# Optimization experiments

Measured on AMD Instinct MI355X. Metric: run time of the kernel, lower is better.

## Reference

```python
import jax, jax.numpy as jnp
import numpy as np

DT_RANK = 64
N_STATES = 16


def selective_scan(u, delta, A, B, C, D):
    # u,delta: [b,l,d]; A: [d,n]; B,C: [b,l,n]; D: [d]
    dA = jnp.einsum('bld,dn->bldn', delta, A)
    dB_u = jnp.einsum('bld,bld,bln->bldn', delta, u, B)
    # shifted exclusive suffix-sum: cum[t] = sum_{s=t+1}^{L-1} dA[s]
    dA_shift = jnp.concatenate([dA[:, 1:], jnp.zeros_like(dA[:, :1])], axis=1)
    dA_cumsum = jnp.exp(jnp.flip(jnp.cumsum(jnp.flip(dA_shift, axis=1), axis=1), axis=1))
    xs = jnp.cumsum(dB_u * dA_cumsum, axis=1) / (dA_cumsum + 1e-12)
    y = jnp.einsum('bldn,bln->bld', xs, C)
    return y + u * D


def setup_inputs() -> dict:
    key = jax.random.key(0)
    ks = jax.random.split(key, 6)
    b, l, d = 2, 1024, 1024
    dt_rank, n = DT_RANK, N_STATES
    x = jax.random.normal(ks[0], (b, l, d), dtype=jnp.float32)
    # Dense kernels with glorot-ish scale
    W_x = jax.random.normal(ks[1], (d, dt_rank + 2 * n), dtype=jnp.float32) * (1.0 / np.sqrt(d))
    W_dt = jax.random.normal(ks[2], (dt_rank, d), dtype=jnp.float32) * (1.0 / np.sqrt(dt_rank))
    b_dt = jnp.zeros((d,), dtype=jnp.float32)
    # A_log = log(repeat(1..n, d)) as in S6.__init__
    A_log = jnp.log(jnp.tile(jnp.arange(1, n + 1, dtype=jnp.float32)[None, :], (d, 1)))
    D = jnp.ones((d,), dtype=jnp.float32)
    W_out = jax.random.normal(ks[3], (d, d), dtype=jnp.float32) * (1.0 / np.sqrt(d))
    b_out = jnp.zeros((d,), dtype=jnp.float32)
    return {"x": x, "W_x": W_x, "W_dt": W_dt, "b_dt": b_dt,
            "A_log": A_log, "D": D, "W_out": W_out, "b_out": b_out}


def reference(x, W_x, W_dt, b_dt, A_log, D, W_out, b_out):
    n = A_log.shape[1]
    A = -jnp.exp(A_log)                     # [d,n]
    x_dbl = jnp.einsum('bld,de->ble', x, W_x)  # [b,l,dt_rank+2n]
    delta = x_dbl[..., :DT_RANK]
    B = x_dbl[..., DT_RANK:DT_RANK + n]
    C = x_dbl[..., DT_RANK + n:]
    delta = jax.nn.softplus(jnp.einsum('blr,rd->bld', delta, W_dt) + b_dt)
    y = selective_scan(x, delta, A, B, C, D)
    return jnp.einsum('bld,de->ble', y, W_out) + b_out
```

## Files before the change

kernel.cpp:

```cpp
#include <hip/hip_runtime.h>
#include <hip/hip_bf16.h>

#define LSEQ 1024
#define DMODEL 1024
#define NSTATE 16
#define DTRANK 64
#define ECOL 96
#define MTOT 2048

typedef short s16x8 __attribute__((ext_vector_type(8)));
typedef float f32x4 __attribute__((ext_vector_type(4)));
typedef unsigned int u32x4 __attribute__((ext_vector_type(4)));

#if __has_builtin(__builtin_amdgcn_exp2f)
#define EXP2F(x) __builtin_amdgcn_exp2f(x)
#else
#define EXP2F(x) exp2f(x)
#endif
#define LOG2E 1.4426950408889634

__device__ inline unsigned short f2bf(float f) {
    unsigned int u = __builtin_bit_cast(unsigned int, f);
    u += 0x7FFFu + ((u >> 16) & 1u);
    return (unsigned short)(u >> 16);
}
__device__ inline float bf2f(unsigned short h) {
    unsigned int u = ((unsigned int)h) << 16;
    return __builtin_bit_cast(float, u);
}

__device__ inline f32x4 shflup4(f32x4 v, int off) {
    f32x4 r;
    r[0] = __shfl_up(v[0], off, 64);
    r[1] = __shfl_up(v[1], off, 64);
    r[2] = __shfl_up(v[2], off, 64);
    r[3] = __shfl_up(v[3], off, 64);
    return r;
}

__global__ __launch_bounds__(256) void k_prep(const float* __restrict__ x,
                                              const float* __restrict__ Wx,
                                              const float* __restrict__ Wdt,
                                              const float* __restrict__ Wout,
                                              unsigned short* __restrict__ xTbf,
                                              unsigned short* __restrict__ WxTh,
                                              unsigned short* __restrict__ WxTl,
                                              unsigned short* __restrict__ WdtTh,
                                              unsigned short* __restrict__ WdtTl,
                                              unsigned short* __restrict__ WbfT) {
    __shared__ float t[64][65];
    int id = blockIdx.x;
    int tid = threadIdx.x;
    if (id < 512) {
        int d0 = (id & 15) * 64, m0 = (id >> 4) * 64;
        int tx = tid & 63, ty = tid >> 6;
#pragma unroll
        for (int j = 0; j < 64; j += 4)
            t[ty + j][tx] = x[(size_t)(m0 + ty + j) * 1024 + d0 + tx];
        __syncthreads();
#pragma unroll
        for (int j = 0; j < 64; j += 4)
            xTbf[(size_t)(d0 + ty + j) * 2048 + m0 + tx] = f2bf(t[tx][ty + j]);
    } else if (id < 512 + 96) {
        int id2 = id - 512;
        int e0 = (id2 % 3) * 32, k0 = (id2 / 3) * 32;
        int tx = tid & 31, ty = tid >> 5;
#pragma unroll
        for (int j = 0; j < 32; j += 8)
            t[ty + j][tx] = Wx[(size_t)(k0 + ty + j) * 96 + e0 + tx];
        __syncthreads();
#pragma unroll
        for (int j = 0; j < 32; j += 8) {
            float v = t[tx][ty + j];
            unsigned short h = f2bf(v);
            WxTh[(size_t)(e0 + ty + j) * 1024 + k0 + tx] = h;
            WxTl[(size_t)(e0 + ty + j) * 1024 + k0 + tx] = f2bf(v - bf2f(h));
        }
    } else if (id < 512 + 96 + 64) {
        int id3 = id - (512 + 96);
        int d0 = (id3 & 31) * 32, r0 = (id3 >> 5) * 32;
        int tx = tid & 31, ty = tid >> 5;
#pragma unroll
        for (int j = 0; j < 32; j += 8)
            t[ty + j][tx] = Wdt[(size_t)(r0 + ty + j) * 1024 + d0 + tx];
        __syncthreads();
#pragma unroll
        for (int j = 0; j < 32; j += 8) {
            float v = t[tx][ty + j];
            unsigned short h = f2bf(v);
            WdtTh[(size_t)(d0 + ty + j) * 64 + r0 + tx] = h;
            WdtTl[(size_t)(d0 + ty + j) * 64 + r0 + tx] = f2bf(v - bf2f(h));
        }
    } else {
        int id4 = id - (512 + 96 + 64);
        int e0 = (id4 & 15) * 64, k0 = (id4 >> 4) * 64;
        int tx = tid & 63, ty = tid >> 6;
#pragma unroll
        for (int j = 0; j < 64; j += 4)
            t[ty + j][tx] = Wout[(size_t)(k0 + ty + j) * 1024 + e0 + tx];
        __syncthreads();
#pragma unroll
        for (int j = 0; j < 64; j += 4)
            WbfT[(size_t)(e0 + ty + j) * 1024 + k0 + tx] = f2bf(t[tx][ty + j]);
    }
}

__global__ __launch_bounds__(256) void k_xdbl3(const float* __restrict__ x,
                                               const unsigned short* __restrict__ WxTh,
                                               const unsigned short* __restrict__ WxTl,
                                               float* __restrict__ part) {
    __shared__ unsigned short Ah[32 * 64], Al[32 * 64];
    __shared__ unsigned short Bh[96 * 64], Bl[96 * 64];
    int bm = (blockIdx.x >> 2) * 32;
    int slice = blockIdx.x & 3;
    int tid = threadIdx.x, lane = tid & 63, w = tid >> 6;
    int wm = w >> 1, wn = w & 1;
    int r = lane & 15, kb = lane >> 4;

    f32x4 acc[3];
#pragma unroll
    for (int nf = 0; nf < 3; ++nf) acc[nf] = (f32x4){0.f, 0.f, 0.f, 0.f};

#pragma unroll 1
    for (int kc = 0; kc < 4; ++kc) {
        int kbase = slice * 256 + kc * 64;
        __syncthreads();
        {
            int row = tid >> 3, cc = tid & 7;
            size_t src = (size_t)(bm + row) * 1024 + kbase + cc * 8;
            float4 v0 = *(const float4*)&x[src];
            float4 v1 = *(const float4*)&x[src + 4];
            float vv[8] = {v0.x, v0.y, v0.z, v0.w, v1.x, v1.y, v1.z, v1.w};
            s16x8 h, lo;
#pragma unroll
            for (int j = 0; j < 8; ++j) {
                unsigned short hb = f2bf(vv[j]);
                h[j] = (short)hb;
                lo[j] = (short)f2bf(vv[j] - bf2f(hb));
            }
            int dstB = row * 128 + ((cc * 16) ^ ((row & 7) << 4));
            *(s16x8*)((char*)Ah + dstB) = h;
            *(s16x8*)((char*)Al + dstB) = lo;
        }
#pragma unroll
        for (int j = 0; j < 3; ++j) {
            int c = tid + j * 256;
            int row = c >> 3, cc = c & 7;
            size_t src = (size_t)row * 1024 + kbase + cc * 8;
            int dstB = row * 128 + ((cc * 16) ^ ((row & 7) << 4));
            *(s16x8*)((char*)Bh + dstB) = *(const s16x8*)&WxTh[src];
            *(s16x8*)((char*)Bl + dstB) = *(const s16x8*)&WxTl[src];
        }
        __syncthreads();
#pragma unroll
        for (int ks = 0; ks < 2; ++ks) {
            int sw = (ks * 64 + kb * 16) ^ ((r & 7) << 4);
            s16x8 a_h = *(const s16x8*)((char*)Ah + (wm * 16 + r) * 128 + sw);
            s16x8 a_l = *(const s16x8*)((char*)Al + (wm * 16 + r) * 128 + sw);
#pragma unroll
            for (int nf = 0; nf < 3; ++nf) {
                int brow = wn * 48 + nf * 16 + r;
                s16x8 b_h = *(const s16x8*)((char*)Bh + brow * 128 + sw);
                s16x8 b_l = *(const s16x8*)((char*)Bl + brow * 128 + sw);
                acc[nf] = __builtin_amdgcn_mfma_f32_16x16x32_bf16(a_h, b_h, acc[nf], 0, 0, 0);
                acc[nf] = __builtin_amdgcn_mfma_f32_16x16x32_bf16(a_h, b_l, acc[nf], 0, 0, 0);
                acc[nf] = __builtin_amdgcn_mfma_f32_16x16x32_bf16(a_l, b_h, acc[nf], 0, 0, 0);
            }
        }
    }
    float* pb = part + (size_t)slice * 2048 * 96;
#pragma unroll
    for (int nf = 0; nf < 3; ++nf)
#pragma unroll
        for (int j = 0; j < 4; ++j)
            pb[(size_t)(bm + wm * 16 + kb * 4 + j) * 96 + wn * 48 + nf * 16 + r] = acc[nf][j];
}

__global__ __launch_bounds__(256) void k_delta2(const float* __restrict__ part,
                                                const unsigned short* __restrict__ WdtTh,
                                                const unsigned short* __restrict__ WdtTl,
                                                const float* __restrict__ bdt,
                                                float* __restrict__ deltaT,
                                                float* __restrict__ bpk,
                                                float* __restrict__ cpk) {
    __shared__ char pool[34816];
    unsigned short* Ah = (unsigned short*)pool;
    unsigned short* Al = (unsigned short*)(pool + 16384);
    float (*slab)[32][68] = (float (*)[32][68])pool;

    int bm = blockIdx.y * 128;
    int bn = blockIdx.x * 64;
    int tid = threadIdx.x, lane = tid & 63, w = tid >> 6;
    int wm = w >> 1, wn = w & 1;
    int r = lane & 15, kb = lane >> 4;

#pragma unroll
    for (int i = 0; i < 8; ++i) {
        int q = tid + i * 256;
        int row = q >> 4, c4 = q & 15;
        size_t off = (size_t)(bm + row) * 96 + c4 * 4;
        f32x4 v = *(const f32x4*)&part[off];
#pragma unroll
        for (int s = 1; s < 4; ++s) v += *(const f32x4*)&part[(size_t)s * 2048 * 96 + off];
        ushort4 h4, l4;
        h4.x = f2bf(v[0]); l4.x = f2bf(v[0] - bf2f(h4.x));
        h4.y = f2bf(v[1]); l4.y = f2bf(v[1] - bf2f(h4.y));
        h4.z = f2bf(v[2]); l4.z = f2bf(v[2] - bf2f(h4.z));
        h4.w = f2bf(v[3]); l4.w = f2bf(v[3] - bf2f(h4.w));
        int dstB = row * 128 + ((c4 * 8) ^ ((row & 7) << 4));
        *(ushort4*)((char*)Ah + dstB) = h4;
        *(ushort4*)((char*)Al + dstB) = l4;
    }
    if (blockIdx.x == 0) {
#pragma unroll
        for (int i = 0; i < 4; ++i) {
            int q = tid + i * 256;
            int row = q >> 3, c4 = q & 7;
            size_t off = (size_t)(bm + row) * 96 + 64 + c4 * 4;
            f32x4 v = *(const f32x4*)&part[off];
#pragma unroll
            for (int s = 1; s < 4; ++s) v += *(const f32x4*)&part[(size_t)s * 2048 * 96 + off];
            if (c4 < 4) *(f32x4*)&bpk[(size_t)(bm + row) * 16 + c4 * 4] = v;
            else        *(f32x4*)&cpk[(size_t)(bm + row) * 16 + (c4 - 4) * 4] = v;
        }
    }
    __syncthreads();

    f32x4 acc[4][2];
#pragma unroll
    for (int mf = 0; mf < 4; ++mf)
#pragma unroll
        for (int nf = 0; nf < 2; ++nf) acc[mf][nf] = (f32x4){0.f, 0.f, 0.f, 0.f};

#pragma unroll
    for (int ks = 0; ks < 2; ++ks) {
        int sw = (ks * 64 + kb * 16) ^ ((r & 7) << 4);
        s16x8 Afh[4], Afl[4], Bh[2], Bl[2];
#pragma unroll
        for (int mf = 0; mf < 4; ++mf) {
            int arow = wm * 64 + mf * 16 + r;
            Afh[mf] = *(const s16x8*)((char*)Ah + arow * 128 + sw);
            Afl[mf] = *(const s16x8*)((char*)Al + arow * 128 + sw);
        }
#pragma unroll
        for (int nf = 0; nf < 2; ++nf) {
            size_t b = (size_t)(bn + wn * 32 + nf * 16 + r) * 64 + ks * 32 + kb * 8;
            Bh[nf] = *(const s16x8*)&WdtTh[b];
            Bl[nf] = *(const s16x8*)&WdtTl[b];
        }
#pragma unroll
        for (int mf = 0; mf < 4; ++mf)
#pragma unroll
            for (int nf = 0; nf < 2; ++nf) {
                acc[mf][nf] = __builtin_amdgcn_mfma_f32_16x16x32_bf16(Afh[mf], Bh[nf], acc[mf][nf], 0, 0, 0);
                acc[mf][nf] = __builtin_amdgcn_mfma_f32_16x16x32_bf16(Afh[mf], Bl[nf], acc[mf][nf], 0, 0, 0);
                acc[mf][nf] = __builtin_amdgcn_mfma_f32_16x16x32_bf16(Afl[mf], Bh[nf], acc[mf][nf], 0, 0, 0);
            }
    }
    __syncthreads();

#pragma unroll
    for (int nf = 0; nf < 2; ++nf) {
        float bb = bdt[bn + wn * 32 + nf * 16 + r];
#pragma unroll
        for (int mf = 0; mf < 4; ++mf)
#pragma unroll
            for (int j = 0; j < 4; ++j) {
                float z = acc[mf][nf][j] + bb;
                float sp = fmaxf(z, 0.f) + log1pf(expf(-fabsf(z)));
                slab[w][nf * 16 + r][mf * 16 + kb * 4 + j] = sp;
            }
    }
#pragma unroll
    for (int i = 0; i < 8; ++i) {
        int idx = i * 64 + lane;
        int dl = idx >> 4, mq = (idx & 15) * 4;
        f32x4 v = *(const f32x4*)&slab[w][dl][mq];
        *(f32x4*)&deltaT[(size_t)(bn + wn * 32 + dl) * MTOT + bm + wm * 64 + mq] = v;
    }
}

__global__ __launch_bounds__(256) void k_scan3(const float* __restrict__ deltaT,
                                               const unsigned short* __restrict__ xTbf,
                                               const float* __restrict__ bpk,
                                               const float* __restrict__ cpk,
                                               const float* __restrict__ Alog,
                                               const float* __restrict__ Dp,
                                               unsigned short* __restrict__ yTbf) {
    __shared__ double csum[64];
    __shared__ double Rbef[64];
    __shared__ float TcL[64 * 20];
    __shared__ float syp[64 * 17];

    int tid = threadIdx.x;
    int c = tid >> 2, l = tid & 3;
    int w = tid >> 6, lane = tid & 63;
    int d = blockIdx.x & 1023, b = blockIdx.x >> 10;
    int m0 = b * 1024;

    const f32x4* dp = (const f32x4*)(deltaT + (size_t)d * MTOT + m0 + c * 16);
    const unsigned short* up = xTbf + (size_t)d * MTOT + m0 + c * 16;
    const f32x4* Bp = (const f32x4*)bpk + (size_t)(m0 + c * 16) * 4 + l;
    const f32x4* Cp = (const f32x4*)cpk + (size_t)(m0 + c * 16) * 4 + l;

    double dsum = 0.0;
#pragma unroll
    for (int i = 0; i < 4; ++i) {
        f32x4 v = dp[i];
        dsum += (double)v[0] + (double)v[1] + (double)v[2] + (double)v[3];
    }
    if (l == 0) csum[c] = dsum;
    __syncthreads();
    if (tid < 64) {
        double v = csum[tid];
#pragma unroll
        for (int off = 1; off < 64; off <<= 1) {
            double t = __shfl_down(v, off, 64);
            if (tid + off < 64) v += t;
        }
        Rbef[tid] = v;
    }
    __syncthreads();

    float Af2[4], Sb2[4];
    double Rb = Rbef[c];
#pragma unroll
    for (int j = 0; j < 4; ++j) {
        float Af = -__expf(Alog[d * NSTATE + 4 * l + j]);
        double A2 = (double)Af * LOG2E;
        Af2[j] = (float)A2;
        Sb2[j] = (float)(A2 * Rb);
    }
    float Dv = Dp[d];

    float P = 0.f;
    f32x4 Tn = {0.f, 0.f, 0.f, 0.f};
#pragma unroll 1
    for (int t4 = 0; t4 < 4; ++t4) {
        f32x4 rdv = dp[t4];
        ushort4 uv = *(const ushort4*)(up + t4 * 4);
        float ru[4] = {bf2f(uv.x), bf2f(uv.y), bf2f(uv.z), bf2f(uv.w)};
        f32x4 Bq[4];
#pragma unroll
        for (int k = 0; k < 4; ++k) Bq[k] = Bp[(t4 * 4 + k) * 4];
#pragma unroll
        for (int k = 0; k < 4; ++k) {
            float dlt = rdv[k];
            P += dlt;
            float du = dlt * ru[k];
#pragma unroll
            for (int j = 0; j < 4; ++j) {
                float e = EXP2F(fmaf(-Af2[j], P, Sb2[j]));
                Tn[j] = fmaf(du * Bq[k][j], e, Tn[j]);
            }
        }
    }
    *(f32x4*)&TcL[c * 20 + 4 * l] = Tn;
    __syncthreads();

    {
        f32x4 v = *(const f32x4*)&TcL[lane * 20 + 4 * w];
#pragma unroll
        for (int off = 1; off < 64; off <<= 1) {
            f32x4 t = shflup4(v, off);
            if (lane >= off) v += t;
        }
        f32x4 ex = shflup4(v, 1);
        if (lane == 0) ex = (f32x4){0.f, 0.f, 0.f, 0.f};
        *(f32x4*)&TcL[lane * 20 + 4 * w] = ex;
    }
    __syncthreads();
    f32x4 num = *(const f32x4*)&TcL[c * 20 + 4 * l];

    P = 0.f;
#pragma unroll 1
    for (int t4 = 0; t4 < 4; ++t4) {
        f32x4 rdv = dp[t4];
        ushort4 uv = *(const ushort4*)(up + t4 * 4);
        float ru[4] = {bf2f(uv.x), bf2f(uv.y), bf2f(uv.z), bf2f(uv.w)};
        f32x4 Bq[4], Cq[4];
#pragma unroll
        for (int k = 0; k < 4; ++k) {
            Bq[k] = Bp[(t4 * 4 + k) * 4];
            Cq[k] = Cp[(t4 * 4 + k) * 4];
        }
#pragma unroll
        for (int k = 0; k < 4; ++k) {
            float dlt = rdv[k];
            P += dlt;
            float du = dlt * ru[k];
            float psum = 0.f;
#pragma unroll
            for (int j = 0; j < 4; ++j) {
                float e = EXP2F(fmaf(-Af2[j], P, Sb2[j]));
                num[j] = fmaf(du * Bq[k][j], e, num[j]);
                float rr = __builtin_amdgcn_rcpf(e + 1e-12f);
                psum = fmaf(num[j] * rr, Cq[k][j], psum);
            }
            psum += __shfl_xor(psum, 1);
            psum += __shfl_xor(psum, 2);
            if (l == 0) syp[c * 17 + t4 * 4 + k] = fmaf(ru[k], Dv, psum);
        }
    }
    __syncthreads();
    {
        int cc = tid >> 2, oo = (tid & 3) * 4;
        const float* sp = &syp[cc * 17 + oo];
        ushort4 o;
        o.x = f2bf(sp[0]);
        o.y = f2bf(sp[1]);
        o.z = f2bf(sp[2]);
        o.w = f2bf(sp[3]);
        *reinterpret_cast<ushort4*>(&yTbf[(size_t)d * MTOT + m0 + tid * 4]) = o;
    }
}

__global__ __launch_bounds__(256) void k_gemm(const unsigned short* __restrict__ yT,
                                              const unsigned short* __restrict__ B,
                                              const float* __restrict__ bias,
                                              float* __restrict__ out) {
    __shared__ unsigned int P[32 * 68];
    __shared__ unsigned short Bs[64 * 64];
    const int GN = 1024, GK = 1024;
    int bm = blockIdx.y * 64;
    int bn = blockIdx.x * 64;
    int tid = threadIdx.x;
    int lane = tid & 63;
    int w = tid >> 6;
    int wm = w >> 1, wn = w & 1;
    int r = lane & 15, kb = lane >> 4;

    f32x4 acc[2][2];
#pragma unroll
    for (int mf = 0; mf < 2; ++mf)
#pragma unroll
        for (int nf = 0; nf < 2; ++nf) acc[mf][nf] = (f32x4){0.f, 0.f, 0.f, 0.f};

    ushort4 rya[2], ryb[2];
    s16x8 rbv[2];
    auto stage_load = [&](int k0) {
#pragma unroll
        for (int i = 0; i < 2; ++i) {
            int slot = tid + i * 256;
            int p = slot >> 4, mq = (slot & 15) * 4;
            rya[i] = *(const ushort4*)&yT[(size_t)(k0 + 2 * p) * MTOT + bm + mq];
            ryb[i] = *(const ushort4*)&yT[(size_t)(k0 + 2 * p + 1) * MTOT + bm + mq];
            rbv[i] = *(const s16x8*)&B[(size_t)(bn + (slot >> 3)) * GK + k0 + (slot & 7) * 8];
        }
    };

    stage_load(0);
    for (int k0 = 0; k0 < GK; k0 += 64) {
        __syncthreads();
#pragma unroll
        for (int i = 0; i < 2; ++i) {
            int slot = tid + i * 256;
            int p = slot >> 4, mq = (slot & 15) * 4;
            u32x4 pk;
            pk[0] = (unsigned int)rya[i].x | ((unsigned int)ryb[i].x << 16);
            pk[1] = (unsigned int)rya[i].y | ((unsigned int)ryb[i].y << 16);
            pk[2] = (unsigned int)rya[i].z | ((unsigned int)ryb[i].z << 16);
            pk[3] = (unsigned int)rya[i].w | ((unsigned int)ryb[i].w << 16);
            *(u32x4*)&P[p * 68 + mq] = pk;
            int row = slot >> 3;
            int dstB = row * 128 + (((slot & 7) * 16) ^ ((row & 7) << 4));
            *(s16x8*)((char*)Bs + dstB) = rbv[i];
        }
        __syncthreads();
        if (k0 + 64 < GK) stage_load(k0 + 64);
#pragma unroll
        for (int ks = 0; ks < 2; ++ks) {
            int sw = (ks * 64 + kb * 16) ^ ((r & 7) << 4);
            s16x8 af[2], bfr[2];
#pragma unroll
            for (int mf = 0; mf < 2; ++mf) {
                int base = (ks * 16 + kb * 4) * 68 + wm * 32 + mf * 16 + r;
                u32x4 av;
                av[0] = P[base];
                av[1] = P[base + 68];
                av[2] = P[base + 136];
                av[3] = P[base + 204];
                af[mf] = __builtin_bit_cast(s16x8, av);
            }
#pragma unroll
            for (int nf = 0; nf < 2; ++nf)
                bfr[nf] = *(const s16x8*)((char*)Bs + (wn * 32 + nf * 16 + r) * 128 + sw);
#pragma unroll
            for (int mf = 0; mf < 2; ++mf)
#pragma unroll
                for (int nf = 0; nf < 2; ++nf)
                    acc[mf][nf] = __builtin_amdgcn_mfma_f32_16x16x32_bf16(af[mf], bfr[nf], acc[mf][nf], 0, 0, 0);
        }
    }
#pragma unroll
    for (int nf = 0; nf < 2; ++nf) {
        float bb = bias[bn + wn * 32 + nf * 16 + r];
#pragma unroll
        for (int mf = 0; mf < 2; ++mf)
#pragma unroll
            for (int j = 0; j < 4; ++j)
                out[(size_t)(bm + wm * 32 + mf * 16 + kb * 4 + j) * GN + bn + wn * 32 + nf * 16 + r] =
                    acc[mf][nf][j] + bb;
    }
}

extern "C" void kernel_launch(void* const* d_in, const int* in_sizes, int n_in,
                              void* d_out, int out_size, void* d_ws, size_t ws_size,
                              hipStream_t stream) {
    const float* x    = (const float*)d_in[0];
    const float* Wx   = (const float*)d_in[1];
    const float* Wdt  = (const float*)d_in[2];
    const float* bdt  = (const float*)d_in[3];
    const float* Alog = (const float*)d_in[4];
    const float* Dp   = (const float*)d_in[5];
    const float* Wout = (const float*)d_in[6];
    const float* bout = (const float*)d_in[7];
    float* out = (float*)d_out;

    float* deltaT = (float*)d_ws;
    float* bpk    = deltaT + 1024 * 2048;
    float* cpk    = bpk + 2048 * 16;
    float* part   = cpk + 2048 * 16;
    unsigned short* xTbf  = (unsigned short*)(part + 4 * 2048 * 96);
    unsigned short* WxTh  = xTbf + 1024 * 2048;
    unsigned short* WxTl  = WxTh + 96 * 1024;
    unsigned short* WdtTh = WxTl + 96 * 1024;
    unsigned short* WdtTl = WdtTh + 1024 * 64;
    unsigned short* yTbf  = WdtTl + 1024 * 64;
    unsigned short* WbfT  = yTbf + 1024 * 2048;

    k_prep<<<928, 256, 0, stream>>>(x, Wx, Wdt, Wout, xTbf,
                                    WxTh, WxTl, WdtTh, WdtTl, WbfT);
    k_xdbl3<<<256, 256, 0, stream>>>(x, WxTh, WxTl, part);
    k_delta2<<<dim3(16, 16), 256, 0, stream>>>(part, WdtTh, WdtTl, bdt, deltaT, bpk, cpk);
    k_scan3<<<2048, 256, 0, stream>>>(deltaT, xTbf, bpk, cpk, Alog, Dp, yTbf);
    k_gemm<<<dim3(16, 32), 256, 0, stream>>>(yTbf, WbfT, bout, out);
}
```

Before: 74.03 us.

## Fold prep transposes into xdbl and delta kernels, convert Wx on the fly

Removes the separate prep kernel. The Wdt and Wout transposes now run as extra blocks of the x_dbl GEMM kernel, and the x transpose to bf16 runs as extra blocks of the delta kernel. The x_dbl GEMM now reads fp32 Wx directly and splits it into bf16 hi/lo inside the tile load, so no pre-transposed Wx buffer is needed. This saves one launch and a workspace round trip. In exchange it adds strided, uncoalesced Wx reads that are repeated across all 256 GEMM blocks.

Result: faster. 65.47 us (-11.6%).

```diff
diff --git a/kernel.cpp b/kernel.cpp
--- a/kernel.cpp
+++ b/kernel.cpp
@@ -38,82 +38,57 @@
     return r;
 }
 
-__global__ __launch_bounds__(256) void k_prep(const float* __restrict__ x,
+__global__ __launch_bounds__(256) void k_xdbl(const float* __restrict__ x,
                                               const float* __restrict__ Wx,
                                               const float* __restrict__ Wdt,
                                               const float* __restrict__ Wout,
-                                              unsigned short* __restrict__ xTbf,
-                                              unsigned short* __restrict__ WxTh,
-                                              unsigned short* __restrict__ WxTl,
+                                              float* __restrict__ part,
                                               unsigned short* __restrict__ WdtTh,
                                               unsigned short* __restrict__ WdtTl,
                                               unsigned short* __restrict__ WbfT) {
-    __shared__ float t[64][65];
-    int id = blockIdx.x;
+    __shared__ alignas(16) char pool[32768];
+    int bid = blockIdx.x;
     int tid = threadIdx.x;
-    if (id < 512) {
-        int d0 = (id & 15) * 64, m0 = (id >> 4) * 64;
-        int tx = tid & 63, ty = tid >> 6;
-#pragma unroll
-        for (int j = 0; j < 64; j += 4)
-            t[ty + j][tx] = x[(size_t)(m0 + ty + j) * 1024 + d0 + tx];
-        __syncthreads();
-#pragma unroll
-        for (int j = 0; j < 64; j += 4)
-            xTbf[(size_t)(d0 + ty + j) * 2048 + m0 + tx] = f2bf(t[tx][ty + j]);
-    } else if (id < 512 + 96) {
-        int id2 = id - 512;
-        int e0 = (id2 % 3) * 32, k0 = (id2 / 3) * 32;
-        int tx = tid & 31, ty = tid >> 5;
-#pragma unroll
-        for (int j = 0; j < 32; j += 8)
-            t[ty + j][tx] = Wx[(size_t)(k0 + ty + j) * 96 + e0 + tx];
-        __syncthreads();
-#pragma unroll
-        for (int j = 0; j < 32; j += 8) {
-            float v = t[tx][ty + j];
-            unsigned short h = f2bf(v);
-            WxTh[(size_t)(e0 + ty + j) * 1024 + k0 + tx] = h;
-            WxTl[(size_t)(e0 + ty + j) * 1024 + k0 + tx] = f2bf(v - bf2f(h));
-        }
-    } else if (id < 512 + 96 + 64) {
-        int id3 = id - (512 + 96);
-        int d0 = (id3 & 31) * 32, r0 = (id3 >> 5) * 32;
-        int tx = tid & 31, ty = tid >> 5;
-#pragma unroll
-        for (int j = 0; j < 32; j += 8)
-            t[ty + j][tx] = Wdt[(size_t)(r0 + ty + j) * 1024 + d0 + tx];
-        __syncthreads();
-#pragma unroll
-        for (int j = 0; j < 32; j += 8) {
-            float v = t[tx][ty + j];
-            unsigned short h = f2bf(v);
-            WdtTh[(size_t)(d0 + ty + j) * 64 + r0 + tx] = h;
-            WdtTl[(size_t)(d0 + ty + j) * 64 + r0 + tx] = f2bf(v - bf2f(h));
-        }
-    } else {
-        int id4 = id - (512 + 96 + 64);
-        int e0 = (id4 & 15) * 64, k0 = (id4 >> 4) * 64;
-        int tx = tid & 63, ty = tid >> 6;
-#pragma unroll
-        for (int j = 0; j < 64; j += 4)
-            t[ty + j][tx] = Wout[(size_t)(k0 + ty + j) * 1024 + e0 + tx];
-        __syncthreads();
-#pragma unroll
-        for (int j = 0; j < 64; j += 4)
-            WbfT[(size_t)(e0 + ty + j) * 1024 + k0 + tx] = f2bf(t[tx][ty + j]);
-    }
-}
-
-__global__ __launch_bounds__(256) void k_xdbl3(const float* __restrict__ x,
-                                               const unsigned short* __restrict__ WxTh,
-                                               const unsigned short* __restrict__ WxTl,
-                                               float* __restrict__ part) {
-    __shared__ unsigned short Ah[32 * 64], Al[32 * 64];
-    __shared__ unsigned short Bh[96 * 64], Bl[96 * 64];
-    int bm = (blockIdx.x >> 2) * 32;
-    int slice = blockIdx.x & 3;
-    int tid = threadIdx.x, lane = tid & 63, w = tid >> 6;
+
+    if (bid >= 256) {
+        float (*t)[65] = (float (*)[65])pool;
+        if (bid < 320) {
+            int id3 = bid - 256;
+            int d0 = (id3 & 31) * 32, r0 = (id3 >> 5) * 32;
+            int tx = tid & 31, ty = tid >> 5;
+#pragma unroll
+            for (int j = 0; j < 32; j += 8)
+                t[ty + j][tx] = Wdt[(size_t)(r0 + ty + j) * 1024 + d0 + tx];
+            __syncthreads();
+#pragma unroll
+            for (int j = 0; j < 32; j += 8) {
+                float v = t[tx][ty + j];
+                unsigned short h = f2bf(v);
+                WdtTh[(size_t)(d0 + ty + j) * 64 + r0 + tx] = h;
+                WdtTl[(size_t)(d0 + ty + j) * 64 + r0 + tx] = f2bf(v - bf2f(h));
+            }
+        } else {
+            int id4 = bid - 320;
+            int e0 = (id4 & 15) * 64, k0 = (id4 >> 4) * 64;
+            int tx = tid & 63, ty = tid >> 6;
+#pragma unroll
+            for (int j = 0; j < 64; j += 4)
+                t[ty + j][tx] = Wout[(size_t)(k0 + ty + j) * 1024 + e0 + tx];
+            __syncthreads();
+#pragma unroll
+            for (int j = 0; j < 64; j += 4)
+                WbfT[(size_t)(e0 + ty + j) * 1024 + k0 + tx] = f2bf(t[tx][ty + j]);
+        }
+        return;
+    }
+
+    unsigned short* Ah = (unsigned short*)pool;
+    unsigned short* Al = (unsigned short*)(pool + 4096);
+    unsigned short* Bh = (unsigned short*)(pool + 8192);
+    unsigned short* Bl = (unsigned short*)(pool + 20480);
+    int bm = (bid >> 2) * 32;
+    int slice = bid & 3;
+    int lane = tid & 63, w = tid >> 6;
     int wm = w >> 1, wn = w & 1;
     int r = lane & 15, kb = lane >> 4;
 
@@ -143,13 +118,21 @@
             *(s16x8*)((char*)Al + dstB) = lo;
         }
 #pragma unroll
-        for (int j = 0; j < 3; ++j) {
-            int c = tid + j * 256;
-            int row = c >> 3, cc = c & 7;
-            size_t src = (size_t)row * 1024 + kbase + cc * 8;
-            int dstB = row * 128 + ((cc * 16) ^ ((row & 7) << 4));
-            *(s16x8*)((char*)Bh + dstB) = *(const s16x8*)&WxTh[src];
-            *(s16x8*)((char*)Bl + dstB) = *(const s16x8*)&WxTl[src];
+        for (int it = 0; it < 3; ++it) {
+            int item = it * 256 + tid;
+            int e = item % 96;
+            int cc = item / 96;
+            s16x8 h, lo;
+#pragma unroll
+            for (int j = 0; j < 8; ++j) {
+                float v = Wx[(size_t)(kbase + cc * 8 + j) * 96 + e];
+                unsigned short hb = f2bf(v);
+                h[j] = (short)hb;
+                lo[j] = (short)f2bf(v - bf2f(hb));
+            }
+            int dstB = e * 128 + ((cc * 16) ^ ((e & 7) << 4));
+            *(s16x8*)((char*)Bh + dstB) = h;
+            *(s16x8*)((char*)Bl + dstB) = lo;
         }
         __syncthreads();
 #pragma unroll
@@ -180,17 +163,37 @@
                                                 const unsigned short* __restrict__ WdtTh,
                                                 const unsigned short* __restrict__ WdtTl,
                                                 const float* __restrict__ bdt,
+                                                const float* __restrict__ x,
                                                 float* __restrict__ deltaT,
                                                 float* __restrict__ bpk,
-                                                float* __restrict__ cpk) {
-    __shared__ char pool[34816];
+                                                float* __restrict__ cpk,
+                                                unsigned short* __restrict__ xTbf) {
+    __shared__ alignas(16) char pool[34816];
+    int bid = blockIdx.x;
+    int tid = threadIdx.x;
+
+    if (bid >= 256) {
+        float (*t)[65] = (float (*)[65])pool;
+        int id = bid - 256;
+        int d0 = (id & 15) * 64, m0 = (id >> 4) * 64;
+        int tx = tid & 63, ty = tid >> 6;
+#pragma unroll
+        for (int j = 0; j < 64; j += 4)
+            t[ty + j][tx] = x[(size_t)(m0 + ty + j) * 1024 + d0 + tx];
+        __syncthreads();
+#pragma unroll
+        for (int j = 0; j < 64; j += 4)
+            xTbf[(size_t)(d0 + ty + j) * 2048 + m0 + tx] = f2bf(t[tx][ty + j]);
+        return;
+    }
+
     unsigned short* Ah = (unsigned short*)pool;
     unsigned short* Al = (unsigned short*)(pool + 16384);
     float (*slab)[32][68] = (float (*)[32][68])pool;
-
-    int bm = blockIdx.y * 128;
-    int bn = blockIdx.x * 64;
-    int tid = threadIdx.x, lane = tid & 63, w = tid >> 6;
+    int bxq = bid & 15, byq = bid >> 4;
+    int bm = byq * 128;
+    int bn = bxq * 64;
+    int lane = tid & 63, w = tid >> 6;
     int wm = w >> 1, wn = w & 1;
     int r = lane & 15, kb = lane >> 4;
 
@@ -211,7 +214,7 @@
         *(ushort4*)((char*)Ah + dstB) = h4;
         *(ushort4*)((char*)Al + dstB) = l4;
     }
-    if (blockIdx.x == 0) {
+    if (bxq == 0) {
 #pragma unroll
         for (int i = 0; i < 4; ++i) {
             int q = tid + i * 256;
@@ -522,17 +525,13 @@
     float* cpk    = bpk + 2048 * 16;
     float* part   = cpk + 2048 * 16;
     unsigned short* xTbf  = (unsigned short*)(part + 4 * 2048 * 96);
-    unsigned short* WxTh  = xTbf + 1024 * 2048;
-    unsigned short* WxTl  = WxTh + 96 * 1024;
-    unsigned short* WdtTh = WxTl + 96 * 1024;
+    unsigned short* WdtTh = xTbf + 1024 * 2048;
     unsigned short* WdtTl = WdtTh + 1024 * 64;
     unsigned short* yTbf  = WdtTl + 1024 * 64;
     unsigned short* WbfT  = yTbf + 1024 * 2048;
 
-    k_prep<<<928, 256, 0, stream>>>(x, Wx, Wdt, Wout, xTbf,
-                                    WxTh, WxTl, WdtTh, WdtTl, WbfT);
-    k_xdbl3<<<256, 256, 0, stream>>>(x, WxTh, WxTl, part);
-    k_delta2<<<dim3(16, 16), 256, 0, stream>>>(part, WdtTh, WdtTl, bdt, deltaT, bpk, cpk);
+    k_xdbl<<<576, 256, 0, stream>>>(x, Wx, Wdt, Wout, part, WdtTh, WdtTl, WbfT);
+    k_delta2<<<768, 256, 0, stream>>>(part, WdtTh, WdtTl, bdt, x, deltaT, bpk, cpk, xTbf);
     k_scan3<<<2048, 256, 0, stream>>>(deltaT, xTbf, bpk, cpk, Alog, Dp, yTbf);
     k_gemm<<<dim3(16, 32), 256, 0, stream>>>(yTbf, WbfT, bout, out);
 }
```
